# Performance work log

Measured on AMD Instinct MI355X. Metric: run time of the kernel, lower is better.

Reference implementation:

```python
import math
import jax, jax.numpy as jnp
import numpy as np

EMB = 1024
NHEADS = 16
CTX = 2048
LN_EPS = 1e-5


def new_gelu(x):
    c = math.sqrt(2.0 / math.pi)
    return 0.5 * x * (1.0 + jnp.tanh(c * (x + 0.044715 * x * x * x)))


def layer_norm(x, g, b):
    mu = jnp.mean(x, axis=-1, keepdims=True)
    var = jnp.mean(jnp.square(x - mu), axis=-1, keepdims=True)
    return (x - mu) * jax.lax.rsqrt(var + LN_EPS) * g + b


def setup_inputs() -> dict:
    key = jax.random.key(0)
    ks = jax.random.split(key, 12)
    s = 0.02
    return {
        "x": jax.random.normal(ks[0], (2, 2048, EMB), dtype=jnp.float32),
        "ln1_g": jnp.ones((EMB,), jnp.float32),
        "ln1_b": jnp.zeros((EMB,), jnp.float32),
        "W_attn": jax.random.normal(ks[1], (EMB, 3 * EMB), jnp.float32) * s,
        "b_attn": jnp.zeros((3 * EMB,), jnp.float32),
        "W_attn_proj": jax.random.normal(ks[2], (EMB, EMB), jnp.float32) * s,
        "b_attn_proj": jnp.zeros((EMB,), jnp.float32),
        "ln2_g": jnp.ones((EMB,), jnp.float32),
        "ln2_b": jnp.zeros((EMB,), jnp.float32),
        "W_fc": jax.random.normal(ks[3], (EMB, 4 * EMB), jnp.float32) * s,
        "b_fc": jnp.zeros((4 * EMB,), jnp.float32),
        "W_mlp_proj": jax.random.normal(ks[4], (4 * EMB, EMB), jnp.float32) * s,
        "b_mlp_proj": jnp.zeros((EMB,), jnp.float32),
    }


def reference(x, ln1_g, ln1_b, W_attn, b_attn, W_attn_proj, b_attn_proj,
              ln2_g, ln2_b, W_fc, b_fc, W_mlp_proj, b_mlp_proj):
    B, S, E = x.shape
    hd = E // NHEADS

    # x = ln_1(x)
    x = layer_norm(x, ln1_g, ln1_b)

    # attention on normalized x
    qkv = x @ W_attn + b_attn                      # [B,S,3E]
    q, k, v = jnp.split(qkv, 3, axis=-1)
    q = q.reshape(B, S, NHEADS, hd).transpose(0, 2, 1, 3)  # [B,H,S,hd]
    k = k.reshape(B, S, NHEADS, hd).transpose(0, 2, 1, 3)
    v = v.reshape(B, S, NHEADS, hd).transpose(0, 2, 1, 3)

    attn = jnp.einsum("bhqd,bhkd->bhqk", q, k) * (1.0 / math.sqrt(hd))
    causal = jnp.tril(jnp.ones((S, S), dtype=bool))
    attn = jnp.where(causal[None, None], attn, -jnp.inf)
    attn = jax.nn.softmax(attn, axis=-1)
    out = jnp.einsum("bhqk,bhkd->bhqd", attn, v)   # [B,H,S,hd]
    out = out.transpose(0, 2, 1, 3).reshape(B, S, E)
    out = out @ W_attn_proj + b_attn_proj

    x = x + out

    # x = ln_2(x)
    x = layer_norm(x, ln2_g, ln2_b)

    # MLP on normalized x
    h = new_gelu(x @ W_fc + b_fc)
    h = h @ W_mlp_proj + b_mlp_proj
    return x + h
```

## Files before the change

### kernel.cpp

```cpp
#include <hip/hip_runtime.h>
#include <cstdint>

typedef __attribute__((ext_vector_type(8))) short bf16x8;
typedef __attribute__((ext_vector_type(4))) float f32x4;
typedef __attribute__((ext_vector_type(16))) float f32x16;
typedef __attribute__((ext_vector_type(4))) unsigned short u16x4;
typedef __attribute__((ext_vector_type(4))) unsigned int u32x4;
typedef unsigned short u16;

#define LOG2E 1.44269504088896340736f

__device__ __forceinline__ u16 f2bf(float f) {
  unsigned u = __builtin_bit_cast(unsigned, f);
  u += 0x7FFFu + ((u >> 16) & 1u);
  return (u16)(u >> 16);
}
__device__ __forceinline__ float bf2f(u16 h) {
  return __builtin_bit_cast(float, ((unsigned)h) << 16);
}

#define GLOAD_LDS16(g, l)                                                              \
  __builtin_amdgcn_global_load_lds((const __attribute__((address_space(1))) void*)(g), \
                                   (__attribute__((address_space(3))) void*)(l), 16, 0, 0)

__global__ __launch_bounds__(256) void k_transpose_bf16(
    const float* __restrict__ W, u16* __restrict__ Wt, int K, int N) {
  __shared__ float tile[32][33];
  const int tid = threadIdx.x;
  const int tx = tid & 31, ty = tid >> 5;
  const int n0 = blockIdx.x * 32, k0 = blockIdx.y * 32;
#pragma unroll
  for (int i = 0; i < 32; i += 8)
    tile[ty + i][tx] = W[(size_t)(k0 + ty + i) * N + n0 + tx];
  __syncthreads();
#pragma unroll
  for (int i = 0; i < 32; i += 8)
    Wt[(size_t)(n0 + ty + i) * K + k0 + tx] = f2bf(tile[tx][ty + i]);
}

__global__ __launch_bounds__(256) void k_layernorm_bf16(
    const float* __restrict__ x, const float* __restrict__ g,
    const float* __restrict__ b, u16* __restrict__ y) {
  const int row = blockIdx.x, tid = threadIdx.x;
  const float4 v = ((const float4*)(x + (size_t)row * 1024))[tid];
  float s = v.x + v.y + v.z + v.w;
#pragma unroll
  for (int m = 1; m < 64; m <<= 1) s += __shfl_xor(s, m);
  __shared__ float ps[8];
  if ((tid & 63) == 0) ps[tid >> 6] = s;
  __syncthreads();
  const float mean = (ps[0] + ps[1] + ps[2] + ps[3]) * (1.0f / 1024.0f);
  const float d0 = v.x - mean, d1 = v.y - mean, d2 = v.z - mean, d3 = v.w - mean;
  float s2 = d0 * d0 + d1 * d1 + d2 * d2 + d3 * d3;
#pragma unroll
  for (int m = 1; m < 64; m <<= 1) s2 += __shfl_xor(s2, m);
  if ((tid & 63) == 0) ps[4 + (tid >> 6)] = s2;
  __syncthreads();
  const float var = (ps[4] + ps[5] + ps[6] + ps[7]) * (1.0f / 1024.0f);
  const float rstd = rsqrtf(var + 1e-5f);
  const float4 gv = ((const float4*)g)[tid];
  const float4 bv = ((const float4*)b)[tid];
  u16x4 o;
  o[0] = f2bf(d0 * rstd * gv.x + bv.x);
  o[1] = f2bf(d1 * rstd * gv.y + bv.y);
  o[2] = f2bf(d2 * rstd * gv.z + bv.z);
  o[3] = f2bf(d3 * rstd * gv.w + bv.w);
  *(u16x4*)(y + (size_t)row * 1024 + tid * 4) = o;
}

__device__ __forceinline__ float gelu_f(float x) {
  const float u = 0.7978845608028654f * (x + 0.044715f * x * x * x);
  const float e = exp2f(u * 2.8853900817779268f);
  const float t = 1.0f - 2.0f / (e + 1.0f);
  return 0.5f * x * (1.0f + t);
}

template <int EPI>
__global__ __launch_bounds__(256, 2) void k_gemm_bt(
    const u16* __restrict__ A, const u16* __restrict__ Bt,
    const float* __restrict__ bias, const u16* __restrict__ resid,
    void* __restrict__ out, u16* __restrict__ vt, int M, int N, int K) {
  __shared__ u16 As[2][128 * 64];
  __shared__ u16 Bs[2][128 * 64];
  const int tid = threadIdx.x;
  const int rowBase = blockIdx.y * 128, colBase = blockIdx.x * 128;
  const int w = tid >> 6, l = tid & 63;
  const int wm = w >> 1, wn = w & 1;
  const int lrow = l & 15, lg = l >> 4;
  const int srow = tid >> 3, sslot = tid & 7;

  const f32x4 fz = {0.f, 0.f, 0.f, 0.f};
  f32x4 acc[4][4];
#pragma unroll
  for (int m = 0; m < 4; m++)
#pragma unroll
    for (int n = 0; n < 4; n++) acc[m][n] = fz;

  const int NT = K >> 6;
  auto STAGE = [&](int b, int kt) {
#pragma unroll
    for (int i = 0; i < 4; i++) {
      const int r = srow + 32 * i;
      const int gs = sslot ^ (r & 7);
      GLOAD_LDS16(A + (size_t)(rowBase + r) * K + kt * 64 + gs * 8,
                  (char*)As[b] + i * 4096 + tid * 16);
      GLOAD_LDS16(Bt + (size_t)(colBase + r) * K + kt * 64 + gs * 8,
                  (char*)Bs[b] + i * 4096 + tid * 16);
    }
  };

  STAGE(0, 0);
  for (int kt = 0; kt < NT; ++kt) {
    const int buf = kt & 1;
    if (kt + 1 < NT) {
      STAGE(buf ^ 1, kt + 1);
      asm volatile("s_waitcnt vmcnt(8)" ::: "memory");
    } else {
      asm volatile("s_waitcnt vmcnt(0)" ::: "memory");
    }
    __builtin_amdgcn_s_barrier();
    const char* Ab = (const char*)As[buf];
    const char* Bb = (const char*)Bs[buf];
#pragma unroll
    for (int kc = 0; kc < 2; kc++) {
      bf16x8 av[4], bv[4];
#pragma unroll
      for (int m = 0; m < 4; m++) {
        const int r = wm * 64 + m * 16 + lrow;
        const int sl = (kc * 4 + lg) ^ (r & 7);
        av[m] = *(const bf16x8*)(Ab + r * 128 + sl * 16);
      }
#pragma unroll
      for (int n = 0; n < 4; n++) {
        const int r = wn * 64 + n * 16 + lrow;
        const int sl = (kc * 4 + lg) ^ (r & 7);
        bv[n] = *(const bf16x8*)(Bb + r * 128 + sl * 16);
      }
#pragma unroll
      for (int m = 0; m < 4; m++)
#pragma unroll
        for (int n = 0; n < 4; n++)
          acc[m][n] = __builtin_amdgcn_mfma_f32_16x16x32_bf16(av[m], bv[n], acc[m][n], 0, 0, 0);
    }
    __builtin_amdgcn_s_barrier();
  }
#pragma unroll
  for (int n = 0; n < 4; n++) {
    const int col = colBase + wn * 64 + n * 16 + lrow;
    const float bval = bias[col];
#pragma unroll
    for (int m = 0; m < 4; m++) {
      const int row0 = rowBase + wm * 64 + m * 16 + lg * 4;
      if (EPI == 3 && col >= 2048) {
        const int c2 = col - 2048;
        const int hh = c2 >> 6, dd = c2 & 63;
        const int bat = row0 >> 11, tok0 = row0 & 2047;
        u16x4 pk;
#pragma unroll
        for (int r = 0; r < 4; r++) pk[r] = f2bf(acc[m][n][r] + bval);
        *(u16x4*)(vt + ((size_t)(bat * 16 + hh) * 64 + dd) * 2048 + tok0) = pk;
      } else if (EPI == 3) {
#pragma unroll
        for (int r = 0; r < 4; r++)
          ((u16*)out)[(size_t)(row0 + r) * 2048 + col] = f2bf(acc[m][n][r] + bval);
      } else {
#pragma unroll
        for (int r = 0; r < 4; r++) {
          const size_t idx = (size_t)(row0 + r) * N + col;
          float v = acc[m][n][r] + bval;
          if (EPI == 0) {
            ((u16*)out)[idx] = f2bf(v);
          } else if (EPI == 2) {
            ((u16*)out)[idx] = f2bf(gelu_f(v));
          } else {
            v += bf2f(resid[idx]);
            ((float*)out)[idx] = v;
          }
        }
      }
    }
  }
}

__global__ __launch_bounds__(256, 2) void k_attention(
    const u16* __restrict__ qk, const u16* __restrict__ VT, u16* __restrict__ out) {
  const int S = 2048, E2 = 2048;
  const int bid = blockIdx.x;
  const int qt = 15 - (bid >> 5);
  const int bh = bid & 31;
  const int bat = bh >> 4, h = bh & 15;
  const u16* base = qk + (size_t)bat * S * E2;
  const u16* kbase = base + 1024 + h * 64;
  const u16* vbase = VT + (size_t)bh * 64 * S;
  const int tid = threadIdx.x, w = tid >> 6, l = tid & 63;
  const int l31 = l & 31, lh = l >> 5;
  __shared__ u16 Ks[2][64 * 64];
  __shared__ u16 Vs[2][64 * 64];
  const int srow = tid >> 3;
  const int gs = (tid & 7) ^ (srow & 7);
  const float sc = 0.125f * LOG2E;
  const float RTHR = 8.0f / sc;

  auto STAGE = [&](int bufi, int kb) {
#pragma unroll
    for (int round = 0; round < 2; round++) {
      const int r = srow + 32 * round;
      GLOAD_LDS16(kbase + (size_t)(kb + r) * E2 + gs * 8, (char*)Ks[bufi] + round * 4096 + tid * 16);
      GLOAD_LDS16(vbase + (size_t)r * S + kb + gs * 8, (char*)Vs[bufi] + round * 4096 + tid * 16);
    }
  };

  const int wq0 = qt * 128 + w * 32;
  const int qg = wq0 + l31;
  const int tdiag = wq0 >> 6;
  const int nkt = 2 * qt + 2;

  bf16x8 qf[4];
#pragma unroll
  for (int s = 0; s < 4; s++)
    qf[s] = *(const bf16x8*)(base + (size_t)qg * E2 + h * 64 + s * 16 + lh * 8);

  f32x16 o0, o1;
#pragma unroll
  for (int r = 0; r < 16; r++) { o0[r] = 0.f; o1[r] = 0.f; }
  float mrow = -1e30f, lsum = 0.f;

  STAGE(0, 0);
  __syncthreads();

  for (int t = 0; t < nkt; t++) {
    const int cur = t & 1;
    const int kb = t * 64;
    if (t + 1 < nkt) STAGE(cur ^ 1, kb + 64);
    if (t <= tdiag) {
      const u16* Kc = Ks[cur];
      const u16* Vc = Vs[cur];

      f32x16 sv0, sv1;
#pragma unroll
      for (int r = 0; r < 16; r++) { sv0[r] = 0.f; sv1[r] = 0.f; }
#pragma unroll
      for (int s = 0; s < 4; s++) {
        const int row0 = l31, row1 = 32 + l31;
        const int sl = s * 2 + lh;
        const bf16x8 k0 = *(const bf16x8*)(Kc + row0 * 64 + ((sl ^ (row0 & 7)) * 8));
        const bf16x8 k1 = *(const bf16x8*)(Kc + row1 * 64 + ((sl ^ (row1 & 7)) * 8));
        sv0 = __builtin_amdgcn_mfma_f32_32x32x16_bf16(k0, qf[s], sv0, 0, 0, 0);
        sv1 = __builtin_amdgcn_mfma_f32_32x32x16_bf16(k1, qf[s], sv1, 0, 0, 0);
      }

      if (t == tdiag) {
#pragma unroll
        for (int reg = 0; reg < 16; reg++) {
          const int kl = (reg & 3) + 8 * (reg >> 2) + 4 * lh;
          if (kb + kl > qg) sv0[reg] = -1e30f;
          if (kb + 32 + kl > qg) sv1[reg] = -1e30f;
        }
      }

      float tmax = sv0[0];
#pragma unroll
      for (int reg = 1; reg < 16; reg++) tmax = fmaxf(tmax, sv0[reg]);
#pragma unroll
      for (int reg = 0; reg < 16; reg++) tmax = fmaxf(tmax, sv1[reg]);
      tmax = fmaxf(tmax, __shfl_xor(tmax, 32));

      if (!__all(tmax - mrow <= RTHR)) {
        const float mnew = fmaxf(mrow, tmax);
        const float corr = exp2f((mrow - mnew) * sc);
        lsum *= corr;
#pragma unroll
        for (int reg = 0; reg < 16; reg++) { o0[reg] *= corr; o1[reg] *= corr; }
        mrow = mnew;
      }
      const float msc = mrow * sc;

      float p0[16], p1[16];
      float rsum = 0.f;
#pragma unroll
      for (int reg = 0; reg < 16; reg++) {
        p0[reg] = exp2f(fmaf(sv0[reg], sc, -msc));
        p1[reg] = exp2f(fmaf(sv1[reg], sc, -msc));
        rsum += p0[reg] + p1[reg];
      }
      rsum += __shfl_xor(rsum, 32);
      lsum += rsum;

      unsigned pk0[8], pk1[8], ex0[8], ex1[8];
#pragma unroll
      for (int j = 0; j < 8; j++) {
        asm("v_cvt_pk_bf16_f32 %0, %1, %2" : "=v"(pk0[j]) : "v"(p0[2 * j]), "v"(p0[2 * j + 1]));
        asm("v_cvt_pk_bf16_f32 %0, %1, %2" : "=v"(pk1[j]) : "v"(p1[2 * j]), "v"(p1[2 * j + 1]));
        ex0[j] = (unsigned)__shfl_xor((int)pk0[j], 32);
        ex1[j] = (unsigned)__shfl_xor((int)pk1[j], 32);
      }
      const bool lo = (lh == 0);

#pragma unroll
      for (int kh = 0; kh < 2; kh++) {
#pragma unroll
        for (int sl2 = 0; sl2 < 2; sl2++) {
          const int ks = kh * 2 + sl2;
          const unsigned* pk = kh ? pk1 : pk0;
          const unsigned* ex = kh ? ex1 : ex0;
          const int j0 = sl2 * 4;
          const unsigned b0 = lo ? pk[j0 + 0] : ex[j0 + 2];
          const unsigned b1 = lo ? pk[j0 + 1] : ex[j0 + 3];
          const unsigned b2 = lo ? ex[j0 + 0] : pk[j0 + 2];
          const unsigned b3 = lo ? ex[j0 + 1] : pk[j0 + 3];
          const u32x4 pbu = {b0, b1, b2, b3};
          const bf16x8 pb = __builtin_bit_cast(bf16x8, pbu);
          const int sl = ks * 2 + lh;
          const int r0 = l31, r1 = 32 + l31;
          const bf16x8 v0 = *(const bf16x8*)(Vc + r0 * 64 + ((sl ^ (r0 & 7)) * 8));
          const bf16x8 v1 = *(const bf16x8*)(Vc + r1 * 64 + ((sl ^ (r1 & 7)) * 8));
          o0 = __builtin_amdgcn_mfma_f32_32x32x16_bf16(v0, pb, o0, 0, 0, 0);
          o1 = __builtin_amdgcn_mfma_f32_32x32x16_bf16(v1, pb, o1, 0, 0, 0);
        }
      }
    }
    __syncthreads();
  }

  const float inv = 1.0f / lsum;
  const size_t orow = (size_t)(bat * S + qg) * 1024 + h * 64;
#pragma unroll
  for (int g = 0; g < 4; g++) {
    u16x4 s0, s1;
#pragma unroll
    for (int r = 0; r < 4; r++) {
      s0[r] = f2bf(o0[4 * g + r] * inv);
      s1[r] = f2bf(o1[4 * g + r] * inv);
    }
    const int d0 = 8 * g + 4 * lh;
    *(u16x4*)(out + orow + d0) = s0;
    *(u16x4*)(out + orow + 32 + d0) = s1;
  }
}

extern "C" void kernel_launch(void* const* d_in, const int* in_sizes, int n_in,
                              void* d_out, int out_size, void* d_ws, size_t ws_size,
                              hipStream_t stream) {
  (void)in_sizes; (void)n_in; (void)out_size; (void)ws_size;
  const float* x      = (const float*)d_in[0];
  const float* ln1_g  = (const float*)d_in[1];
  const float* ln1_b  = (const float*)d_in[2];
  const float* W_attn = (const float*)d_in[3];
  const float* b_attn = (const float*)d_in[4];
  const float* W_proj = (const float*)d_in[5];
  const float* b_proj = (const float*)d_in[6];
  const float* ln2_g  = (const float*)d_in[7];
  const float* ln2_b  = (const float*)d_in[8];
  const float* W_fc   = (const float*)d_in[9];
  const float* b_fc   = (const float*)d_in[10];
  const float* W_mlp  = (const float*)d_in[11];
  const float* b_mlp  = (const float*)d_in[12];

  const int M = 4096;
  char* ws = (char*)d_ws;
  size_t off = 0;
  auto alloc = [&](size_t bytes) {
    void* p = ws + off;
    off += (bytes + 255) & ~(size_t)255;
    return p;
  };
  u16* WattnT = (u16*)alloc((size_t)3072 * 1024 * 2);
  u16* WprojT = (u16*)alloc((size_t)1024 * 1024 * 2);
  u16* WfcT   = (u16*)alloc((size_t)4096 * 1024 * 2);
  u16* WmlpT  = (u16*)alloc((size_t)1024 * 4096 * 2);
  u16* x1     = (u16*)alloc((size_t)M * 1024 * 2);
  u16* qkb    = (u16*)alloc((size_t)M * 2048 * 2);
  u16* VT     = (u16*)alloc((size_t)32 * 64 * 2048 * 2);
  u16* attno  = (u16*)alloc((size_t)M * 1024 * 2);
  float* x2   = (float*)alloc((size_t)M * 1024 * 4);
  u16* x3     = (u16*)alloc((size_t)M * 1024 * 2);
  u16* hbuf   = (u16*)alloc((size_t)M * 4096 * 2);

  const dim3 blk(256);
  k_transpose_bf16<<<dim3(3072 / 32, 1024 / 32), blk, 0, stream>>>(W_attn, WattnT, 1024, 3072);
  k_transpose_bf16<<<dim3(1024 / 32, 1024 / 32), blk, 0, stream>>>(W_proj, WprojT, 1024, 1024);
  k_transpose_bf16<<<dim3(4096 / 32, 1024 / 32), blk, 0, stream>>>(W_fc, WfcT, 1024, 4096);
  k_transpose_bf16<<<dim3(1024 / 32, 4096 / 32), blk, 0, stream>>>(W_mlp, WmlpT, 4096, 1024);

  k_layernorm_bf16<<<M, blk, 0, stream>>>(x, ln1_g, ln1_b, x1);
  k_gemm_bt<3><<<dim3(3072 / 128, M / 128), blk, 0, stream>>>(
      x1, WattnT, b_attn, nullptr, qkb, VT, M, 3072, 1024);
  k_attention<<<dim3(512), blk, 0, stream>>>(qkb, VT, attno);
  k_gemm_bt<1><<<dim3(1024 / 128, M / 128), blk, 0, stream>>>(
      attno, WprojT, b_proj, x1, x2, nullptr, M, 1024, 1024);
  k_layernorm_bf16<<<M, blk, 0, stream>>>(x2, ln2_g, ln2_b, x3);
  k_gemm_bt<2><<<dim3(4096 / 128, M / 128), blk, 0, stream>>>(
      x3, WfcT, b_fc, nullptr, hbuf, nullptr, M, 4096, 1024);
  k_gemm_bt<1><<<dim3(1024 / 128, M / 128), blk, 0, stream>>>(
      hbuf, WmlpT, b_mlp, x3, d_out, nullptr, M, 1024, 4096);
}
```

Baseline: 266.4 us.

## Single-buffer GEMM LDS, raise occupancy, add XCD-aware block swizzle and 64-wide N tiles

The GEMM kernel drops the LDS double buffer in favour of a single buffer with __syncthreads, which halves shared memory so launch bounds can ask for 4 blocks per CU. It also remaps a 1D grid with an XCD-style swizzle so that neighbouring tiles land on the same chiplet for L2 reuse. The N=1024 projection GEMMs switch to 128x64 tiles to roughly double their block count. The trade-off is that global loads no longer overlap with MFMA inside a block, so the kernel now depends on other resident blocks to hide memory latency.

```diff
diff --git a/kernel.cpp b/kernel.cpp
--- a/kernel.cpp
+++ b/kernel.cpp
@@ -75,82 +75,80 @@
   return 0.5f * x * (1.0f + t);
 }
 
-template <int EPI>
-__global__ __launch_bounds__(256, 2) void k_gemm_bt(
+template <int EPI, int BN>
+__global__ __launch_bounds__(256, 4) void k_gemm_bt(
     const u16* __restrict__ A, const u16* __restrict__ Bt,
     const float* __restrict__ bias, const u16* __restrict__ resid,
-    void* __restrict__ out, u16* __restrict__ vt, int M, int N, int K) {
-  __shared__ u16 As[2][128 * 64];
-  __shared__ u16 Bs[2][128 * 64];
+    void* __restrict__ out, u16* __restrict__ vt, int M, int N, int K, int nbx) {
+  constexpr int BM = 128;
+  __shared__ u16 As[BM * 64];
+  __shared__ u16 Bs[BN * 64];
   const int tid = threadIdx.x;
-  const int rowBase = blockIdx.y * 128, colBase = blockIdx.x * 128;
+  const int wg = ((blockIdx.x & 7) * (gridDim.x >> 3)) + (blockIdx.x >> 3);
+  const int bx = wg % nbx, by = wg / nbx;
+  const int rowBase = by * BM, colBase = bx * BN;
   const int w = tid >> 6, l = tid & 63;
-  const int wm = w >> 1, wn = w & 1;
+  const int wm = (BN == 128) ? (w >> 1) : w;
+  const int wn = (BN == 128) ? (w & 1) : 0;
+  constexpr int MR = (BN == 128) ? 4 : 2;
+  constexpr int WROWS = (BN == 128) ? 64 : 32;
   const int lrow = l & 15, lg = l >> 4;
   const int srow = tid >> 3, sslot = tid & 7;
 
   const f32x4 fz = {0.f, 0.f, 0.f, 0.f};
-  f32x4 acc[4][4];
-#pragma unroll
-  for (int m = 0; m < 4; m++)
+  f32x4 acc[MR][4];
+#pragma unroll
+  for (int m = 0; m < MR; m++)
 #pragma unroll
     for (int n = 0; n < 4; n++) acc[m][n] = fz;
 
   const int NT = K >> 6;
-  auto STAGE = [&](int b, int kt) {
-#pragma unroll
-    for (int i = 0; i < 4; i++) {
+  for (int kt = 0; kt < NT; ++kt) {
+#pragma unroll
+    for (int i = 0; i < BM / 32; i++) {
       const int r = srow + 32 * i;
       const int gs = sslot ^ (r & 7);
       GLOAD_LDS16(A + (size_t)(rowBase + r) * K + kt * 64 + gs * 8,
-                  (char*)As[b] + i * 4096 + tid * 16);
+                  (char*)As + i * 4096 + tid * 16);
+    }
+#pragma unroll
+    for (int i = 0; i < BN / 32; i++) {
+      const int r = srow + 32 * i;
+      const int gs = sslot ^ (r & 7);
       GLOAD_LDS16(Bt + (size_t)(colBase + r) * K + kt * 64 + gs * 8,
-                  (char*)Bs[b] + i * 4096 + tid * 16);
-    }
-  };
-
-  STAGE(0, 0);
-  for (int kt = 0; kt < NT; ++kt) {
-    const int buf = kt & 1;
-    if (kt + 1 < NT) {
-      STAGE(buf ^ 1, kt + 1);
-      asm volatile("s_waitcnt vmcnt(8)" ::: "memory");
-    } else {
-      asm volatile("s_waitcnt vmcnt(0)" ::: "memory");
-    }
-    __builtin_amdgcn_s_barrier();
-    const char* Ab = (const char*)As[buf];
-    const char* Bb = (const char*)Bs[buf];
+                  (char*)Bs + i * 4096 + tid * 16);
+    }
+    __syncthreads();
 #pragma unroll
     for (int kc = 0; kc < 2; kc++) {
-      bf16x8 av[4], bv[4];
-#pragma unroll
-      for (int m = 0; m < 4; m++) {
-        const int r = wm * 64 + m * 16 + lrow;
+      bf16x8 av[MR], bv[4];
+#pragma unroll
+      for (int m = 0; m < MR; m++) {
+        const int r = wm * WROWS + m * 16 + lrow;
         const int sl = (kc * 4 + lg) ^ (r & 7);
-        av[m] = *(const bf16x8*)(Ab + r * 128 + sl * 16);
+        av[m] = *(const bf16x8*)((const char*)As + r * 128 + sl * 16);
       }
 #pragma unroll
       for (int n = 0; n < 4; n++) {
         const int r = wn * 64 + n * 16 + lrow;
         const int sl = (kc * 4 + lg) ^ (r & 7);
-        bv[n] = *(const bf16x8*)(Bb + r * 128 + sl * 16);
-      }
-#pragma unroll
-      for (int m = 0; m < 4; m++)
+        bv[n] = *(const bf16x8*)((const char*)Bs + r * 128 + sl * 16);
+      }
+#pragma unroll
+      for (int m = 0; m < MR; m++)
 #pragma unroll
         for (int n = 0; n < 4; n++)
           acc[m][n] = __builtin_amdgcn_mfma_f32_16x16x32_bf16(av[m], bv[n], acc[m][n], 0, 0, 0);
     }
-    __builtin_amdgcn_s_barrier();
+    __syncthreads();
   }
 #pragma unroll
   for (int n = 0; n < 4; n++) {
     const int col = colBase + wn * 64 + n * 16 + lrow;
     const float bval = bias[col];
 #pragma unroll
-    for (int m = 0; m < 4; m++) {
-      const int row0 = rowBase + wm * 64 + m * 16 + lg * 4;
+    for (int m = 0; m < MR; m++) {
+      const int row0 = rowBase + wm * WROWS + m * 16 + lg * 4;
       if (EPI == 3 && col >= 2048) {
         const int c2 = col - 2048;
         const int hh = c2 >> 6, dd = c2 & 63;
@@ -383,14 +381,14 @@
   k_transpose_bf16<<<dim3(1024 / 32, 4096 / 32), blk, 0, stream>>>(W_mlp, WmlpT, 4096, 1024);
 
   k_layernorm_bf16<<<M, blk, 0, stream>>>(x, ln1_g, ln1_b, x1);
-  k_gemm_bt<3><<<dim3(3072 / 128, M / 128), blk, 0, stream>>>(
-      x1, WattnT, b_attn, nullptr, qkb, VT, M, 3072, 1024);
+  k_gemm_bt<3, 128><<<dim3(768), blk, 0, stream>>>(
+      x1, WattnT, b_attn, nullptr, qkb, VT, M, 3072, 1024, 24);
   k_attention<<<dim3(512), blk, 0, stream>>>(qkb, VT, attno);
-  k_gemm_bt<1><<<dim3(1024 / 128, M / 128), blk, 0, stream>>>(
-      attno, WprojT, b_proj, x1, x2, nullptr, M, 1024, 1024);
+  k_gemm_bt<1, 64><<<dim3(512), blk, 0, stream>>>(
+      attno, WprojT, b_proj, x1, x2, nullptr, M, 1024, 1024, 16);
   k_layernorm_bf16<<<M, blk, 0, stream>>>(x2, ln2_g, ln2_b, x3);
-  k_gemm_bt<2><<<dim3(4096 / 128, M / 128), blk, 0, stream>>>(
-      x3, WfcT, b_fc, nullptr, hbuf, nullptr, M, 4096, 1024);
-  k_gemm_bt<1><<<dim3(1024 / 128, M / 128), blk, 0, stream>>>(
-      hbuf, WmlpT, b_mlp, x3, d_out, nullptr, M, 1024, 4096);
-}
+  k_gemm_bt<2, 128><<<dim3(1024), blk, 0, stream>>>(
+      x3, WfcT, b_fc, nullptr, hbuf, nullptr, M, 4096, 1024, 32);
+  k_gemm_bt<1, 64><<<dim3(512), blk, 0, stream>>>(
+      hbuf, WmlpT, b_mlp, x3, d_out, nullptr, M, 1024, 4096, 16);
+}
```

After: 252.6 us. 1.05x faster.
